# Optimization experiments

Hardware: AMD Instinct MI355X
Metric: run time of the kernel (lower is better)

The kernel has to match this reference:

```python
import jax, jax.numpy as jnp
import numpy as np

N = 500_000
N_ATOMS = 5
T = 8                # angle triplets per (residue, bead) table row
CONT_LEN = 36
GATE_OFFSET = 1
NUM_EXPERTS = 18
BEAD_COL = 36
MAX_BEADS = 4
ANGLE_WEIGHT = 1.0
EPS = 1e-8
MIN_LEN = 0.02


def setup_inputs() -> dict:
    key = jax.random.key(0)
    ks = jax.random.split(key, 8)
    x = jax.random.uniform(ks[0], (N, 38), dtype=jnp.float32)
    # gate column holds residue id in [1, num_experts]; bead column in [0, max_beads)
    res = jax.random.randint(ks[1], (N,), 1, NUM_EXPERTS + 1).astype(jnp.float32)
    bead = jax.random.randint(ks[2], (N,), 0, MAX_BEADS).astype(jnp.float32)
    x = x.at[:, CONT_LEN + 1].set(res)
    x = x.at[:, BEAD_COL].set(bead)
    y_true = jax.random.normal(ks[3], (N, N_ATOMS * 3), dtype=jnp.float32)
    y_pred = jax.random.normal(ks[4], (N, N_ATOMS * 3), dtype=jnp.float32)
    mask = (jax.random.uniform(ks[5], (N, N_ATOMS * 3)) < 0.85).astype(jnp.float32)
    # -1 entries act as invalid-triplet sentinels (trip_ok branch)
    trip = jax.random.randint(ks[6], (NUM_EXPERTS, MAX_BEADS, T, 3), -1, N_ATOMS, dtype=jnp.int32)
    valid = jax.random.randint(ks[7], (NUM_EXPERTS, MAX_BEADS, T), 0, 2, dtype=jnp.int32)
    return {"x": x, "y_true": y_true, "y_pred": y_pred, "mask": mask,
            "angle_triplets_table": trip, "angle_valid_table": valid}


def _atom_mse(true, pred, m):
    # masked per-atom squared error, normalized by count of valid atoms per sample
    se_atom = jnp.sum(jnp.square(true - pred) * m, axis=-1)          # [N, A]
    atom_valid = jnp.any(m > 0.0, axis=-1).astype(se_atom.dtype)     # [N, A]
    num = jnp.sum(se_atom * atom_valid, axis=-1)
    den = jnp.sum(atom_valid, axis=-1) + EPS
    return jnp.mean(num / den)


def _angle_loss(x, true, pred, m, trip_table, valid_table):
    gate = x[:, CONT_LEN + 1]
    gate = jnp.where(jnp.isfinite(gate), gate, 0.0)
    res_id = jnp.clip(jnp.round(gate).astype(jnp.int32) - GATE_OFFSET, 0, NUM_EXPERTS - 1)
    bead = x[:, BEAD_COL]
    bead = jnp.where(jnp.isfinite(bead), bead, 0.0)
    bead_id = jnp.clip(jnp.round(bead).astype(jnp.int32), 0, MAX_BEADS - 1)

    atom_valid = jnp.any(m > 0.0, axis=-1)                           # [N, A]
    trip = trip_table[res_id, bead_id]                               # [N, T, 3]
    base_valid = valid_table[res_id, bead_id]                        # [N, T]
    trip_ok = jnp.all(trip >= 0, axis=-1)
    ts = jnp.maximum(trip, 0)
    i_idx, j_idx, k_idx = ts[..., 0], ts[..., 1], ts[..., 2]         # [N, T]

    rows = jnp.arange(true.shape[0])[:, None]
    vi = atom_valid[rows, i_idx]
    vj = atom_valid[rows, j_idx]
    vk = atom_valid[rows, k_idx]
    ti, tj, tk = true[rows, i_idx], true[rows, j_idx], true[rows, k_idx]   # [N, T, 3]
    pi, pj, pk = pred[rows, i_idx], pred[rows, j_idx], pred[rows, k_idx]

    v1t, v2t, v1p, v2p = ti - tj, tk - tj, pi - pj, pk - pj
    ml2 = jnp.float32(MIN_LEN * MIN_LEN)
    sq = lambda v: jnp.sum(jnp.square(v), axis=-1)
    l1t2, l2t2, l1p2, l2p2 = sq(v1t), sq(v2t), sq(v1p), sq(v2p)

    valid = (trip_ok & (base_valid > 0) & vi & vj & vk
             & (l1t2 > ml2) & (l2t2 > ml2) & (l1p2 > ml2) & (l2p2 > ml2))

    unit = lambda v, l2: v * jax.lax.rsqrt(jnp.maximum(l2, ml2))[..., None]
    u1t, u2t = unit(v1t, l1t2), unit(v2t, l2t2)
    u1p, u2p = unit(v1p, l1p2), unit(v2p, l2p2)

    clip = lambda c: jnp.clip(c, -1.0 + 1e-6, 1.0 - 1e-6)
    cos_t = clip(jnp.sum(u1t * u2t, axis=-1))
    cos_p = clip(jnp.sum(u1p * u2p, axis=-1))
    sin_t = jnp.linalg.norm(jnp.cross(u1t, u2t), axis=-1)
    sin_p = jnp.linalg.norm(jnp.cross(u1p, u2p), axis=-1)

    per_ang = jnp.square(cos_p - cos_t) + jnp.square(sin_p - sin_t)
    per_ang = jnp.where(valid, per_ang, 0.0)
    num = jnp.sum(per_ang, axis=-1)
    den = jnp.sum(valid.astype(jnp.float32), axis=-1) + EPS
    return jnp.mean(num / den)


def reference(x, y_true, y_pred, mask, angle_triplets_table, angle_valid_table):
    true = y_true.reshape(-1, N_ATOMS, 3).astype(jnp.float32)
    pred = y_pred.reshape(-1, N_ATOMS, 3).astype(jnp.float32)
    m = mask.reshape(-1, N_ATOMS, 3).astype(jnp.float32)
    atom = _atom_mse(true, pred, m)
    ang = _angle_loss(x, true, pred, m, angle_triplets_table, angle_valid_table)
    return atom + ANGLE_WEIGHT * ang
```

## Files before the change

kernel.cpp:

```cpp
#include <hip/hip_runtime.h>
#include <math.h>

#define NATOMS 5
#define NEXP 18
#define NBEAD 4
#define EPSV 1e-8f
#define ML2 (0.02f * 0.02f)

typedef float vf4a __attribute__((ext_vector_type(4), aligned(16)));
typedef float vf2u __attribute__((ext_vector_type(2), aligned(4)));

__global__ void pack_tables(const int* __restrict__ trip, const int* __restrict__ valid,
                            int4* __restrict__ ptbl) {
    int c = blockIdx.x * blockDim.x + threadIdx.x;
    if (c < NEXP * NBEAD) {
        unsigned w[4] = {0u, 0u, 0u, 0u};
#pragma unroll
        for (int t = 0; t < 8; t++) {
            int b = c * 8 + t;
            int i = trip[b * 3 + 0], j = trip[b * 3 + 1], k = trip[b * 3 + 2];
            unsigned ok = (i >= 0 && j >= 0 && k >= 0 && valid[b] > 0) ? 1u : 0u;
            unsigned oi = 3u * (unsigned)min(max(i, 0), NATOMS - 1);
            unsigned oj = 3u * (unsigned)min(max(j, 0), NATOMS - 1);
            unsigned ov = 3u * (unsigned)min(max(k, 0), NATOMS - 1);
            unsigned e = oi | (oj << 4) | (ov << 8) | (ok << 12);
            w[t >> 1] |= e << ((t & 1) * 16);
        }
        ptbl[c] = make_int4((int)w[0], (int)w[1], (int)w[2], (int)w[3]);
    }
}

__global__ __launch_bounds__(64) void loss_kernel(
    const float* __restrict__ xin, const float* __restrict__ y_true,
    const float* __restrict__ y_pred, const float* __restrict__ mask,
    const int4* __restrict__ ptbl, float* __restrict__ partial, int n) {
    __shared__ float sT[960];
    __shared__ float sP[960];
    __shared__ float sM[960];

    const int tid = threadIdx.x;
    const int rbase = blockIdx.x * 64;
    const int row = rbase + tid;
    const size_t dbase = (size_t)rbase * 15;
    const long long total = (long long)n * 15;

    vf2u gb;
    gb.x = 0.f; gb.y = 0.f;
    if (row < n) gb = __builtin_nontemporal_load((const vf2u*)(xin + (size_t)row * 38 + 36));

    const vf4a* qT = (const vf4a*)(y_true + dbase);
    const vf4a* qP = (const vf4a*)(y_pred + dbase);
    const vf4a* qM = (const vf4a*)(mask + dbase);
    vf4a tC[4], pC[4], mC[4];
    bool ok[4];
#pragma unroll
    for (int k = 0; k < 4; k++) {
        int q = k * 64 + tid;
        ok[k] = (q < 240) && (dbase + 4 * (long long)q + 4 <= total);
        if (ok[k]) {
            tC[k] = __builtin_nontemporal_load(qT + q);
            pC[k] = __builtin_nontemporal_load(qP + q);
            mC[k] = __builtin_nontemporal_load(qM + q);
        }
    }
#pragma unroll
    for (int k = 0; k < 4; k++) {
        int q = k * 64 + tid;
        if (ok[k]) {
            ((vf4a*)sT)[q] = tC[k];
            ((vf4a*)sP)[q] = pC[k];
            ((vf4a*)sM)[q] = mC[k];
        }
    }
    __syncthreads();

    float result = 0.f;
    if (row < n) {
        const float* st = sT + tid * 15;
        const float* sp = sP + tid * 15;
        const float* sm = sM + tid * 15;

        unsigned mrow = 0u;
#pragma unroll
        for (int c = 0; c < 15; c++) mrow |= (sm[c] > 0.f ? 1u : 0u) << c;

        float num_a = 0.f, den_a = 0.f;
        unsigned avm2 = 0u;
#pragma unroll
        for (int a = 0; a < 5; a++) {
            unsigned mb = (mrow >> (3 * a)) & 7u;
            float d0 = st[3 * a + 0] - sp[3 * a + 0];
            float d1 = st[3 * a + 1] - sp[3 * a + 1];
            float d2 = st[3 * a + 2] - sp[3 * a + 2];
            float se = (mb & 1u ? d0 * d0 : 0.f) + (mb & 2u ? d1 * d1 : 0.f) +
                       (mb & 4u ? d2 * d2 : 0.f);
            if (mb) { num_a += se; den_a += 1.f; avm2 |= 1u << (3 * a); }
        }
        result = num_a / (den_a + EPSV);

        float beadf = isfinite(gb.x) ? gb.x : 0.f;
        float gatef = isfinite(gb.y) ? gb.y : 0.f;
        gatef = fminf(fmaxf(gatef, -1e6f), 1e6f);
        beadf = fminf(fmaxf(beadf, -1e6f), 1e6f);
        int rid = min(max((int)rintf(gatef) - 1, 0), NEXP - 1);
        int bid = min(max((int)rintf(beadf), 0), NBEAD - 1);
        int4 pk = ptbl[rid * NBEAD + bid];
        unsigned tw0 = (unsigned)pk.x, tw1 = (unsigned)pk.y;
        unsigned tw2 = (unsigned)pk.z, tw3 = (unsigned)pk.w;

        float num_g = 0.f, den_g = 0.f;
#pragma unroll
        for (int t = 0; t < 8; t++) {
            unsigned wrd = (t < 2) ? tw0 : (t < 4) ? tw1 : (t < 6) ? tw2 : tw3;
            unsigned e = (wrd >> ((t & 1) * 16)) & 0xffffu;
            int oi = e & 15, oj = (e >> 4) & 15, ov = (e >> 8) & 15;
            bool wok = ((e >> 12) & 1u) != 0u;

            float tix = st[oi], tiy = st[oi + 1], tiz = st[oi + 2];
            float tjx = st[oj], tjy = st[oj + 1], tjz = st[oj + 2];
            float tkx = st[ov], tky = st[ov + 1], tkz = st[ov + 2];
            float pix = sp[oi], piy = sp[oi + 1], piz = sp[oi + 2];
            float pjx = sp[oj], pjy = sp[oj + 1], pjz = sp[oj + 2];
            float pkx = sp[ov], pky = sp[ov + 1], pkz = sp[ov + 2];

            float v1tx = tix - tjx, v1ty = tiy - tjy, v1tz = tiz - tjz;
            float v2tx = tkx - tjx, v2ty = tky - tjy, v2tz = tkz - tjz;
            float v1px = pix - pjx, v1py = piy - pjy, v1pz = piz - pjz;
            float v2px = pkx - pjx, v2py = pky - pjy, v2pz = pkz - pjz;

            float l1t = fmaf(v1tx, v1tx, fmaf(v1ty, v1ty, v1tz * v1tz));
            float l2t = fmaf(v2tx, v2tx, fmaf(v2ty, v2ty, v2tz * v2tz));
            float l1p = fmaf(v1px, v1px, fmaf(v1py, v1py, v1pz * v1pz));
            float l2p = fmaf(v2px, v2px, fmaf(v2py, v2py, v2pz * v2pz));

            bool okv = wok && ((avm2 >> oi) & 1) && ((avm2 >> oj) & 1) &&
                       ((avm2 >> ov) & 1) && (l1t > ML2) && (l2t > ML2) &&
                       (l1p > ML2) && (l2p > ML2);

            float rt = __builtin_amdgcn_rsqf(fmaxf(l1t, ML2) * fmaxf(l2t, ML2));
            float rp = __builtin_amdgcn_rsqf(fmaxf(l1p, ML2) * fmaxf(l2p, ML2));

            float dott = fmaf(v1tx, v2tx, fmaf(v1ty, v2ty, v1tz * v2tz));
            float dotp = fmaf(v1px, v2px, fmaf(v1py, v2py, v1pz * v2pz));
            float cut = dott * rt;
            float cup = dotp * rp;
            float cost = fminf(fmaxf(cut, -1.f + 1e-6f), 1.f - 1e-6f);
            float cosp = fminf(fmaxf(cup, -1.f + 1e-6f), 1.f - 1e-6f);
            float sint = __builtin_amdgcn_sqrtf(fmaxf(fmaf(-cut, cut, 1.f), 0.f));
            float sinp = __builtin_amdgcn_sqrtf(fmaxf(fmaf(-cup, cup, 1.f), 0.f));

            float dc = cosp - cost, dsn = sinp - sint;
            if (okv) { num_g += fmaf(dc, dc, dsn * dsn); den_g += 1.f; }
        }
        result += num_g / (den_g + EPSV);
    }

#pragma unroll
    for (int off = 32; off > 0; off >>= 1)
        result += __shfl_down(result, off, 64);
    if (tid == 0) partial[blockIdx.x] = result;
}

__global__ __launch_bounds__(256) void reduce_kernel(const float* __restrict__ partial,
                                                     float* __restrict__ out, int nblocks,
                                                     float inv_n) {
    __shared__ float red[4];
    float s = 0.f;
    for (int i = threadIdx.x; i < nblocks; i += 256) s += partial[i];
#pragma unroll
    for (int off = 32; off > 0; off >>= 1) s += __shfl_down(s, off, 64);
    int lane = threadIdx.x & 63, wv = threadIdx.x >> 6;
    if (lane == 0) red[wv] = s;
    __syncthreads();
    if (threadIdx.x == 0) out[0] = (red[0] + red[1] + red[2] + red[3]) * inv_n;
}

extern "C" void kernel_launch(void* const* d_in, const int* in_sizes, int n_in,
                              void* d_out, int out_size, void* d_ws, size_t ws_size,
                              hipStream_t stream) {
    const float* x = (const float*)d_in[0];
    const float* y_true = (const float*)d_in[1];
    const float* y_pred = (const float*)d_in[2];
    const float* mask = (const float*)d_in[3];
    const int* trip = (const int*)d_in[4];
    const int* valid = (const int*)d_in[5];
    float* out = (float*)d_out;

    int4* ptbl = (int4*)d_ws;
    float* partial = (float*)((char*)d_ws + 4096);

    const int n = in_sizes[1] / 15;
    const int blocks = (n + 63) / 64;

    pack_tables<<<1, 128, 0, stream>>>(trip, valid, ptbl);
    loss_kernel<<<blocks, 64, 0, stream>>>(x, y_true, y_pred, mask, ptbl, partial, n);
    reduce_kernel<<<1, 256, 0, stream>>>(partial, out, blocks, 1.0f / (float)n);
}
```

Measured before the change: 187.0 us.

## Make loss kernel persistent with per-wave tiles and register prefetch

Swaps the one-block-per-64-rows launch for a fixed grid of 512 blocks of four waves. Each wave walks 64-row tiles in a grid-stride loop and prefetches the next tile into registers while computing the current one from its own LDS slice. The aim is to hide global load latency and cut the block launch and partial-sum count, so the final reduce reads 2048 partials instead of thousands. The cost is more register pressure from the prefetch buffers, and a fixed grid size that may leave some compute units underused.

```diff
diff --git a/kernel.cpp b/kernel.cpp
--- a/kernel.cpp
+++ b/kernel.cpp
@@ -9,6 +9,9 @@
 
 typedef float vf4a __attribute__((ext_vector_type(4), aligned(16)));
 typedef float vf2u __attribute__((ext_vector_type(2), aligned(4)));
+
+#define NBLOCKS 512
+#define NWAVES (NBLOCKS * 4)
 
 __global__ void pack_tables(const int* __restrict__ trip, const int* __restrict__ valid,
                             int4* __restrict__ ptbl) {
@@ -30,143 +33,166 @@
     }
 }
 
-__global__ __launch_bounds__(64) void loss_kernel(
-    const float* __restrict__ xin, const float* __restrict__ y_true,
-    const float* __restrict__ y_pred, const float* __restrict__ mask,
-    const int4* __restrict__ ptbl, float* __restrict__ partial, int n) {
-    __shared__ float sT[960];
-    __shared__ float sP[960];
-    __shared__ float sM[960];
-
-    const int tid = threadIdx.x;
-    const int rbase = blockIdx.x * 64;
-    const int row = rbase + tid;
-    const size_t dbase = (size_t)rbase * 15;
-    const long long total = (long long)n * 15;
-
-    vf2u gb;
-    gb.x = 0.f; gb.y = 0.f;
-    if (row < n) gb = __builtin_nontemporal_load((const vf2u*)(xin + (size_t)row * 38 + 36));
-
+__device__ __forceinline__ void load_tile(int t, int lane, long long totald, int n,
+                                          const float* __restrict__ y_true,
+                                          const float* __restrict__ y_pred,
+                                          const float* __restrict__ mask,
+                                          const float* __restrict__ xin,
+                                          vf4a* __restrict__ bT, vf4a* __restrict__ bP,
+                                          vf4a* __restrict__ bM, vf2u& g) {
+    const long long dbase = (long long)t * 960;
+    const int row = t * 64 + lane;
+    if (row < n) g = __builtin_nontemporal_load((const vf2u*)(xin + (size_t)row * 38 + 36));
     const vf4a* qT = (const vf4a*)(y_true + dbase);
     const vf4a* qP = (const vf4a*)(y_pred + dbase);
     const vf4a* qM = (const vf4a*)(mask + dbase);
-    vf4a tC[4], pC[4], mC[4];
-    bool ok[4];
 #pragma unroll
     for (int k = 0; k < 4; k++) {
-        int q = k * 64 + tid;
-        ok[k] = (q < 240) && (dbase + 4 * (long long)q + 4 <= total);
-        if (ok[k]) {
-            tC[k] = __builtin_nontemporal_load(qT + q);
-            pC[k] = __builtin_nontemporal_load(qP + q);
-            mC[k] = __builtin_nontemporal_load(qM + q);
+        int q = k * 64 + lane;
+        if (q < 240 && dbase + 4 * (long long)q + 4 <= totald) {
+            bT[k] = __builtin_nontemporal_load(qT + q);
+            bP[k] = __builtin_nontemporal_load(qP + q);
+            bM[k] = __builtin_nontemporal_load(qM + q);
         }
     }
-#pragma unroll
-    for (int k = 0; k < 4; k++) {
-        int q = k * 64 + tid;
-        if (ok[k]) {
-            ((vf4a*)sT)[q] = tC[k];
-            ((vf4a*)sP)[q] = pC[k];
-            ((vf4a*)sM)[q] = mC[k];
-        }
-    }
-    __syncthreads();
+}
+
+__global__ __launch_bounds__(256, 2) void loss_kernel(
+    const float* __restrict__ xin, const float* __restrict__ y_true,
+    const float* __restrict__ y_pred, const float* __restrict__ mask,
+    const int4* __restrict__ ptbl, float* __restrict__ partial, int n, int ntiles) {
+    __shared__ float sT[4][960];
+    __shared__ float sP[4][960];
+    __shared__ float sM[4][960];
+
+    const int tid = threadIdx.x;
+    const int lane = tid & 63;
+    const int wv = tid >> 6;
+    const int wgid = blockIdx.x * 4 + wv;
+    const long long totald = (long long)n * 15;
+    float* wT = sT[wv];
+    float* wP = sP[wv];
+    float* wM = sM[wv];
 
     float result = 0.f;
-    if (row < n) {
-        const float* st = sT + tid * 15;
-        const float* sp = sP + tid * 15;
-        const float* sm = sM + tid * 15;
-
-        unsigned mrow = 0u;
-#pragma unroll
-        for (int c = 0; c < 15; c++) mrow |= (sm[c] > 0.f ? 1u : 0u) << c;
-
-        float num_a = 0.f, den_a = 0.f;
-        unsigned avm2 = 0u;
-#pragma unroll
-        for (int a = 0; a < 5; a++) {
-            unsigned mb = (mrow >> (3 * a)) & 7u;
-            float d0 = st[3 * a + 0] - sp[3 * a + 0];
-            float d1 = st[3 * a + 1] - sp[3 * a + 1];
-            float d2 = st[3 * a + 2] - sp[3 * a + 2];
-            float se = (mb & 1u ? d0 * d0 : 0.f) + (mb & 2u ? d1 * d1 : 0.f) +
-                       (mb & 4u ? d2 * d2 : 0.f);
-            if (mb) { num_a += se; den_a += 1.f; avm2 |= 1u << (3 * a); }
-        }
-        result = num_a / (den_a + EPSV);
-
-        float beadf = isfinite(gb.x) ? gb.x : 0.f;
-        float gatef = isfinite(gb.y) ? gb.y : 0.f;
-        gatef = fminf(fmaxf(gatef, -1e6f), 1e6f);
-        beadf = fminf(fmaxf(beadf, -1e6f), 1e6f);
-        int rid = min(max((int)rintf(gatef) - 1, 0), NEXP - 1);
-        int bid = min(max((int)rintf(beadf), 0), NBEAD - 1);
-        int4 pk = ptbl[rid * NBEAD + bid];
-        unsigned tw0 = (unsigned)pk.x, tw1 = (unsigned)pk.y;
-        unsigned tw2 = (unsigned)pk.z, tw3 = (unsigned)pk.w;
-
-        float num_g = 0.f, den_g = 0.f;
-#pragma unroll
-        for (int t = 0; t < 8; t++) {
-            unsigned wrd = (t < 2) ? tw0 : (t < 4) ? tw1 : (t < 6) ? tw2 : tw3;
-            unsigned e = (wrd >> ((t & 1) * 16)) & 0xffffu;
-            int oi = e & 15, oj = (e >> 4) & 15, ov = (e >> 8) & 15;
-            bool wok = ((e >> 12) & 1u) != 0u;
-
-            float tix = st[oi], tiy = st[oi + 1], tiz = st[oi + 2];
-            float tjx = st[oj], tjy = st[oj + 1], tjz = st[oj + 2];
-            float tkx = st[ov], tky = st[ov + 1], tkz = st[ov + 2];
-            float pix = sp[oi], piy = sp[oi + 1], piz = sp[oi + 2];
-            float pjx = sp[oj], pjy = sp[oj + 1], pjz = sp[oj + 2];
-            float pkx = sp[ov], pky = sp[ov + 1], pkz = sp[ov + 2];
-
-            float v1tx = tix - tjx, v1ty = tiy - tjy, v1tz = tiz - tjz;
-            float v2tx = tkx - tjx, v2ty = tky - tjy, v2tz = tkz - tjz;
-            float v1px = pix - pjx, v1py = piy - pjy, v1pz = piz - pjz;
-            float v2px = pkx - pjx, v2py = pky - pjy, v2pz = pkz - pjz;
-
-            float l1t = fmaf(v1tx, v1tx, fmaf(v1ty, v1ty, v1tz * v1tz));
-            float l2t = fmaf(v2tx, v2tx, fmaf(v2ty, v2ty, v2tz * v2tz));
-            float l1p = fmaf(v1px, v1px, fmaf(v1py, v1py, v1pz * v1pz));
-            float l2p = fmaf(v2px, v2px, fmaf(v2py, v2py, v2pz * v2pz));
-
-            bool okv = wok && ((avm2 >> oi) & 1) && ((avm2 >> oj) & 1) &&
-                       ((avm2 >> ov) & 1) && (l1t > ML2) && (l2t > ML2) &&
-                       (l1p > ML2) && (l2p > ML2);
-
-            float rt = __builtin_amdgcn_rsqf(fmaxf(l1t, ML2) * fmaxf(l2t, ML2));
-            float rp = __builtin_amdgcn_rsqf(fmaxf(l1p, ML2) * fmaxf(l2p, ML2));
-
-            float dott = fmaf(v1tx, v2tx, fmaf(v1ty, v2ty, v1tz * v2tz));
-            float dotp = fmaf(v1px, v2px, fmaf(v1py, v2py, v1pz * v2pz));
-            float cut = dott * rt;
-            float cup = dotp * rp;
-            float cost = fminf(fmaxf(cut, -1.f + 1e-6f), 1.f - 1e-6f);
-            float cosp = fminf(fmaxf(cup, -1.f + 1e-6f), 1.f - 1e-6f);
-            float sint = __builtin_amdgcn_sqrtf(fmaxf(fmaf(-cut, cut, 1.f), 0.f));
-            float sinp = __builtin_amdgcn_sqrtf(fmaxf(fmaf(-cup, cup, 1.f), 0.f));
-
-            float dc = cosp - cost, dsn = sinp - sint;
-            if (okv) { num_g += fmaf(dc, dc, dsn * dsn); den_g += 1.f; }
-        }
-        result += num_g / (den_g + EPSV);
+    vf4a bT[4], bP[4], bM[4];
+    vf2u g;
+    g.x = 0.f; g.y = 0.f;
+
+    int t = wgid;
+    if (t < ntiles)
+        load_tile(t, lane, totald, n, y_true, y_pred, mask, xin, bT, bP, bM, g);
+
+    for (; t < ntiles; t += NWAVES) {
+#pragma unroll
+        for (int k = 0; k < 4; k++) {
+            int q = k * 64 + lane;
+            if (q < 240 && (long long)t * 960 + 4 * (long long)q + 4 <= totald) {
+                ((vf4a*)wT)[q] = bT[k];
+                ((vf4a*)wP)[q] = bP[k];
+                ((vf4a*)wM)[q] = bM[k];
+            }
+        }
+        const vf2u gcur = g;
+        const int row = t * 64 + lane;
+
+        int tn = t + NWAVES;
+        if (tn < ntiles)
+            load_tile(tn, lane, totald, n, y_true, y_pred, mask, xin, bT, bP, bM, g);
+
+        if (row < n) {
+            const float* st = wT + lane * 15;
+            const float* sp = wP + lane * 15;
+            const float* sm = wM + lane * 15;
+
+            unsigned mrow = 0u;
+#pragma unroll
+            for (int c = 0; c < 15; c++) mrow |= (sm[c] > 0.f ? 1u : 0u) << c;
+
+            float num_a = 0.f, den_a = 0.f;
+            unsigned avm2 = 0u;
+#pragma unroll
+            for (int a = 0; a < 5; a++) {
+                unsigned mb = (mrow >> (3 * a)) & 7u;
+                float d0 = st[3 * a + 0] - sp[3 * a + 0];
+                float d1 = st[3 * a + 1] - sp[3 * a + 1];
+                float d2 = st[3 * a + 2] - sp[3 * a + 2];
+                float se = (mb & 1u ? d0 * d0 : 0.f) + (mb & 2u ? d1 * d1 : 0.f) +
+                           (mb & 4u ? d2 * d2 : 0.f);
+                if (mb) { num_a += se; den_a += 1.f; avm2 |= 1u << (3 * a); }
+            }
+            result += num_a / (den_a + EPSV);
+
+            float beadf = isfinite(gcur.x) ? gcur.x : 0.f;
+            float gatef = isfinite(gcur.y) ? gcur.y : 0.f;
+            gatef = fminf(fmaxf(gatef, -1e6f), 1e6f);
+            beadf = fminf(fmaxf(beadf, -1e6f), 1e6f);
+            int rid = min(max((int)rintf(gatef) - 1, 0), NEXP - 1);
+            int bid = min(max((int)rintf(beadf), 0), NBEAD - 1);
+            int4 pk = ptbl[rid * NBEAD + bid];
+            unsigned tw0 = (unsigned)pk.x, tw1 = (unsigned)pk.y;
+            unsigned tw2 = (unsigned)pk.z, tw3 = (unsigned)pk.w;
+
+            float num_g = 0.f, den_g = 0.f;
+#pragma unroll
+            for (int tt = 0; tt < 8; tt++) {
+                unsigned wrd = (tt < 2) ? tw0 : (tt < 4) ? tw1 : (tt < 6) ? tw2 : tw3;
+                unsigned e = (wrd >> ((tt & 1) * 16)) & 0xffffu;
+                int oi = e & 15, oj = (e >> 4) & 15, ov = (e >> 8) & 15;
+                bool wok = ((e >> 12) & 1u) != 0u;
+
+                float tix = st[oi], tiy = st[oi + 1], tiz = st[oi + 2];
+                float tjx = st[oj], tjy = st[oj + 1], tjz = st[oj + 2];
+                float tkx = st[ov], tky = st[ov + 1], tkz = st[ov + 2];
+                float pix = sp[oi], piy = sp[oi + 1], piz = sp[oi + 2];
+                float pjx = sp[oj], pjy = sp[oj + 1], pjz = sp[oj + 2];
+                float pkx = sp[ov], pky = sp[ov + 1], pkz = sp[ov + 2];
+
+                float v1tx = tix - tjx, v1ty = tiy - tjy, v1tz = tiz - tjz;
+                float v2tx = tkx - tjx, v2ty = tky - tjy, v2tz = tkz - tjz;
+                float v1px = pix - pjx, v1py = piy - pjy, v1pz = piz - pjz;
+                float v2px = pkx - pjx, v2py = pky - pjy, v2pz = pkz - pjz;
+
+                float l1t = fmaf(v1tx, v1tx, fmaf(v1ty, v1ty, v1tz * v1tz));
+                float l2t = fmaf(v2tx, v2tx, fmaf(v2ty, v2ty, v2tz * v2tz));
+                float l1p = fmaf(v1px, v1px, fmaf(v1py, v1py, v1pz * v1pz));
+                float l2p = fmaf(v2px, v2px, fmaf(v2py, v2py, v2pz * v2pz));
+
+                bool okv = wok && ((avm2 >> oi) & 1) && ((avm2 >> oj) & 1) &&
+                           ((avm2 >> ov) & 1) && (l1t > ML2) && (l2t > ML2) &&
+                           (l1p > ML2) && (l2p > ML2);
+
+                float rt = __builtin_amdgcn_rsqf(fmaxf(l1t, ML2) * fmaxf(l2t, ML2));
+                float rp = __builtin_amdgcn_rsqf(fmaxf(l1p, ML2) * fmaxf(l2p, ML2));
+
+                float dott = fmaf(v1tx, v2tx, fmaf(v1ty, v2ty, v1tz * v2tz));
+                float dotp = fmaf(v1px, v2px, fmaf(v1py, v2py, v1pz * v2pz));
+                float cut = dott * rt;
+                float cup = dotp * rp;
+                float cost = fminf(fmaxf(cut, -1.f + 1e-6f), 1.f - 1e-6f);
+                float cosp = fminf(fmaxf(cup, -1.f + 1e-6f), 1.f - 1e-6f);
+                float sint = __builtin_amdgcn_sqrtf(fmaxf(fmaf(-cut, cut, 1.f), 0.f));
+                float sinp = __builtin_amdgcn_sqrtf(fmaxf(fmaf(-cup, cup, 1.f), 0.f));
+
+                float dc = cosp - cost, dsn = sinp - sint;
+                if (okv) { num_g += fmaf(dc, dc, dsn * dsn); den_g += 1.f; }
+            }
+            result += num_g / (den_g + EPSV);
+        }
     }
 
 #pragma unroll
     for (int off = 32; off > 0; off >>= 1)
         result += __shfl_down(result, off, 64);
-    if (tid == 0) partial[blockIdx.x] = result;
+    if (lane == 0) partial[wgid] = result;
 }
 
 __global__ __launch_bounds__(256) void reduce_kernel(const float* __restrict__ partial,
-                                                     float* __restrict__ out, int nblocks,
+                                                     float* __restrict__ out, int m,
                                                      float inv_n) {
     __shared__ float red[4];
     float s = 0.f;
-    for (int i = threadIdx.x; i < nblocks; i += 256) s += partial[i];
+    for (int i = threadIdx.x; i < m; i += 256) s += partial[i];
 #pragma unroll
     for (int off = 32; off > 0; off >>= 1) s += __shfl_down(s, off, 64);
     int lane = threadIdx.x & 63, wv = threadIdx.x >> 6;
@@ -190,9 +216,10 @@
     float* partial = (float*)((char*)d_ws + 4096);
 
     const int n = in_sizes[1] / 15;
-    const int blocks = (n + 63) / 64;
+    const int ntiles = (n + 63) / 64;
 
     pack_tables<<<1, 128, 0, stream>>>(trip, valid, ptbl);
-    loss_kernel<<<blocks, 64, 0, stream>>>(x, y_true, y_pred, mask, ptbl, partial, n);
-    reduce_kernel<<<1, 256, 0, stream>>>(partial, out, blocks, 1.0f / (float)n);
-}
+    loss_kernel<<<NBLOCKS, 256, 0, stream>>>(x, y_true, y_pred, mask, ptbl, partial, n,
+                                             ntiles);
+    reduce_kernel<<<1, 256, 0, stream>>>(partial, out, NWAVES, 1.0f / (float)n);
+}
```

After: 181.8 us. 1.03x faster.
